# Kernel optimization log

Measured on AMD Instinct MI355X. Metric: run time of the kernel, lower is better.

Reference implementation:

```python
import jax, jax.numpy as jnp
import numpy as np
from jax import lax

B, T, LAT, F2, H = 128, 512, 256, 64, 512
D_IN1 = LAT + F2  # gru5 input dim = 320


def hard_sigmoid(x):
    return jnp.clip(0.2 * x + 0.5, 0.0, 1.0)


def gru_seq(x, W, U, b_in, b_rec, hidden):
    """Keras GRU, reset_after=True, tanh / hard_sigmoid, return_sequences.
    x: [B,T,D], W: [D,3H], U: [H,3H], b_in/b_rec: [3H] -> [B,T,H]."""
    xW = jnp.einsum('btd,dk->btk', x, W) + b_in  # [B,T,3H]
    h0 = jnp.zeros((x.shape[0], hidden), x.dtype)

    def step(h, xt):  # xt: [B,3H]
        inner = h @ U + b_rec
        iz, ir, ih = jnp.split(inner, 3, axis=-1)
        xz, xr, xh = jnp.split(xt, 3, axis=-1)
        zg = hard_sigmoid(xz + iz)
        rg = hard_sigmoid(xr + ir)
        hh = jnp.tanh(xh + rg * ih)
        h_new = zg * h + (1.0 - zg) * hh
        return h_new, h_new

    _, hs = lax.scan(step, h0, jnp.swapaxes(xW, 0, 1))  # [T,B,H]
    return jnp.swapaxes(hs, 0, 1)


def setup_inputs() -> dict:
    key = jax.random.key(0)
    ks = jax.random.split(key, 14)
    s = lambda fan: 1.0 / np.sqrt(fan)
    return {
        'z': jax.random.normal(ks[0], (B, LAT), jnp.float32),
        'train_input_two': jax.random.normal(ks[1], (B, T, F2), jnp.float32),
        'masks': jax.random.uniform(ks[2], (B, T, 1), jnp.float32),
        'dec_masks': jax.random.uniform(ks[3], (B, T, 1), jnp.float32),
        'W5': jax.random.normal(ks[4], (D_IN1, 3 * H), jnp.float32) * s(D_IN1),
        'U5': jax.random.normal(ks[5], (H, 3 * H), jnp.float32) * s(H),
        'bi5': jnp.zeros((3 * H,), jnp.float32),
        'br5': jnp.zeros((3 * H,), jnp.float32),
        'W6': jax.random.normal(ks[6], (H, 3 * H), jnp.float32) * s(H),
        'U6': jax.random.normal(ks[7], (H, 3 * H), jnp.float32) * s(H),
        'bi6': jnp.zeros((3 * H,), jnp.float32),
        'br6': jnp.zeros((3 * H,), jnp.float32),
        'Wd': jax.random.normal(ks[8], (H, 1), jnp.float32) * s(H),
        'bd': jnp.zeros((1,), jnp.float32),
    }


def reference(z, train_input_two, masks, dec_masks,
              W5, U5, bi5, br5, W6, U6, bi6, br6, Wd, bd):
    # RepeatVector: [B,LAT] -> [B,T,LAT]
    rep = jnp.broadcast_to(z[:, None, :], (z.shape[0], T, z.shape[1]))
    concat = jnp.concatenate([rep, train_input_two], axis=-1)  # [B,T,LAT+F2]
    masked = concat * masks                                     # CustomMasking
    g5 = gru_seq(masked, W5, U5, bi5, br5, H)                   # [B,T,H]
    g6 = gru_seq(g5, W6, U6, bi6, br6, H)                       # [B,T,H]
    dec = jnp.tanh(jnp.einsum('bth,ho->bto', g6, Wd) + bd)      # TimeDistributed Dense(1, tanh)
    return dec * dec_masks                                      # [B,T,1]
```

## Files before the change

### kernel.cpp

```cpp
#include <hip/hip_runtime.h>
#include <hip/hip_bf16.h>

typedef unsigned short u16;
typedef unsigned int u32;
typedef unsigned long long u64;
typedef __attribute__((ext_vector_type(8))) short bf16x8;
typedef __attribute__((ext_vector_type(4))) float f32x4;

#define MFMA(a,b,c) __builtin_amdgcn_mfma_f32_16x16x32_bf16((a),(b),(c),0,0,0)
#define AGENT __HIP_MEMORY_SCOPE_AGENT


__device__ __forceinline__ u16 f2bf(float f) {
    u32 u = __float_as_uint(f);
    u32 r = (u + 0x7fffu + ((u >> 16) & 1u)) >> 16;
    return (u16)r;
}
__device__ __forceinline__ float bf2f(u16 v) { return __uint_as_float(((u32)v) << 16); }
__device__ __forceinline__ float sat01(float x) { return fminf(1.f, fmaxf(0.f, x)); }
__device__ __forceinline__ float ftanh(float x) {
    x = fminf(10.f, fmaxf(-10.f, x));
    float e = __expf(2.f * x);
    return (e - 1.f) / (e + 1.f);
}

__device__ __forceinline__ bf16x8 loadB(const float* __restrict__ M, int k0, int colbase,
                                        int l15, int q8) {
    const float* p = M + (size_t)(k0 + q8) * 1536 + colbase + l15;
    bf16x8 r;
#pragma unroll
    for (int j = 0; j < 8; ++j) r[j] = (short)f2bf(p[(size_t)j * 1536]);
    return r;
}

__device__ __forceinline__ bf16x8 ldsA(const u16* s, int stride, int colbase, int l15, int q8) {
    return *(const bf16x8*)(s + l15 * stride + colbase + q8);
}

__global__ void zero_ws_kernel(u32* ws) {
    int i = blockIdx.x * 256 + threadIdx.x;
    if (i < 262400) ws[i] = 0u;
}

__global__ void __launch_bounds__(256, 1)
gru_fused(const float* __restrict__ zin, const float* __restrict__ x2,
          const float* __restrict__ msk, const float* __restrict__ dmsk,
          const float* __restrict__ W5, const float* __restrict__ U5,
          const float* __restrict__ bi5, const float* __restrict__ br5,
          const float* __restrict__ W6, const float* __restrict__ U6,
          const float* __restrict__ bi6, const float* __restrict__ br6,
          const float* __restrict__ Wd, const float* __restrict__ bdp,
          float* __restrict__ out, u32* __restrict__ h5w,
          u32* __restrict__ h6w, u32* __restrict__ cc5)
{
    const int wg = blockIdx.x;
    const bool is6 = wg >= 128;
    const int id = is6 ? wg - 128 : wg;
    const int slice = id & 15;
    const int rgp = id >> 4;
    const int row0 = rgp << 4;
    const int sb = slice << 5;
    const int tid = threadIdx.x;
    const int wv = tid >> 6, lane = tid & 63;
    const int l15 = lane & 15, q8 = (lane >> 4) << 3;

    __shared__ u16 stg[16 * 1032];
    __shared__ float exch[8 * 16 * 17];

    const int ct = wv & 1;
    const int gMain = (wv < 2) ? 0 : 1;
    const int colMain = gMain * 512 + sb + ct * 16;
    const int colH = 1024 + sb + ct * 16;

    const float* bi = is6 ? bi6 : bi5;
    const float* br = is6 ? br6 : br5;
    const float biasM = bi[colMain + l15] + br[colMain + l15];
    const float biasS = (wv < 2) ? bi[colH + l15] : br[colH + l15];

    bf16x8 Bm[32], Bs[16];
    if (!is6) {
#pragma unroll
        for (int kt = 0; kt < 10; ++kt) Bm[kt] = loadB(W5, kt * 32, colMain, l15, q8);
#pragma unroll
        for (int kt = 0; kt < 16; ++kt) Bm[10 + kt] = loadB(U5, kt * 32, colMain, l15, q8);
        if (wv < 2) {
#pragma unroll
            for (int kt = 0; kt < 10; ++kt) Bs[kt] = loadB(W5, kt * 32, colH, l15, q8);
        } else {
#pragma unroll
            for (int kt = 0; kt < 16; ++kt) Bs[kt] = loadB(U5, kt * 32, colH, l15, q8);
        }
    } else {
#pragma unroll
        for (int kt = 0; kt < 16; ++kt) Bm[kt] = loadB(W6, kt * 32, colMain, l15, q8);
#pragma unroll
        for (int kt = 0; kt < 16; ++kt) Bm[16 + kt] = loadB(U6, kt * 32, colMain, l15, q8);
        if (wv < 2) {
#pragma unroll
            for (int kt = 0; kt < 16; ++kt) Bs[kt] = loadB(W6, kt * 32, colH, l15, q8);
        } else {
#pragma unroll
            for (int kt = 0; kt < 16; ++kt) Bs[kt] = loadB(U6, kt * 32, colH, l15, q8);
        }
    }

    float wdv[8]; float bdv = 0.f;
    if (is6 && wv == 0) {
#pragma unroll
        for (int j = 0; j < 8; ++j) wdv[j] = Wd[lane * 8 + j];
        bdv = bdp[0];
    }

    float hold0 = 0.f, hold1 = 0.f;
    const int grow = tid >> 4, cp = tid & 15;
    const int c2p = cp >> 3, ccb = (cp & 7) * 2;

    const int r_ = tid >> 4, cth = tid & 15;
    const int b_ = row0 + r_;

    for (int t = 0; t < 514; ++t) {
        if (!is6) {
            if (t < 512) {
                float mk = msk[b_ * 512 + t];
                for (int c = cth; c < 320; c += 16) {
                    float v = (c < 256) ? zin[b_ * 256 + c]
                                        : x2[(b_ * 512 + t) * 64 + (c - 256)];
                    stg[r_ * 840 + c] = f2bf(v * mk);
                }
                {
                    const u64* src = (const u64*)(h5w + ((t + 1) & 1) * 65536 +
                                                  (size_t)b_ * 512);
                    const u32 exp = (u32)t;
                    u64 v[16];
                    while (true) {
                        bool ok = true;
#pragma unroll
                        for (int k = 0; k < 16; ++k)
                            v[k] = __hip_atomic_load(&src[cth + 16 * k], __ATOMIC_RELAXED, AGENT);
#pragma unroll
                        for (int k = 0; k < 16; ++k) {
                            u32 lo = (u32)v[k], hi = (u32)(v[k] >> 32);
                            if (((lo >> 16) != exp) | ((hi >> 16) != exp)) ok = false;
                        }
                        if (ok) break;
                        __builtin_amdgcn_s_sleep(1);
                    }
                    u16* dst = &stg[r_ * 840 + 320];
#pragma unroll
                    for (int k = 0; k < 16; ++k) {
                        u32 lo = (u32)v[k], hi = (u32)(v[k] >> 32);
                        int c = (cth + 16 * k) * 2;
                        *(u32*)&dst[c] = (lo & 0xffffu) | (hi << 16);
                    }
                }
                __syncthreads();
                f32x4 a0 = {biasM, biasM, biasM, biasM};
                f32x4 a1 = {biasS, biasS, biasS, biasS};
                if (wv < 2) {
#pragma unroll
                    for (int kt = 0; kt < 10; ++kt) {
                        bf16x8 a = ldsA(stg, 840, kt * 32, l15, q8);
                        a0 = MFMA(a, Bm[kt], a0);
                        a1 = MFMA(a, Bs[kt], a1);
                    }
#pragma unroll
                    for (int kt = 0; kt < 16; ++kt) {
                        bf16x8 a = ldsA(stg, 840, 320 + kt * 32, l15, q8);
                        a0 = MFMA(a, Bm[10 + kt], a0);
                    }
                } else {
#pragma unroll
                    for (int kt = 0; kt < 10; ++kt) {
                        bf16x8 a = ldsA(stg, 840, kt * 32, l15, q8);
                        a0 = MFMA(a, Bm[kt], a0);
                    }
#pragma unroll
                    for (int kt = 0; kt < 16; ++kt) {
                        bf16x8 a = ldsA(stg, 840, 320 + kt * 32, l15, q8);
                        a0 = MFMA(a, Bm[10 + kt], a0);
                        a1 = MFMA(a, Bs[kt], a1);
                    }
                }
                {
                    int uM = gMain * 2 + ct, uS = (wv < 2 ? 4 + ct : 6 + ct);
#pragma unroll
                    for (int i = 0; i < 4; ++i) {
                        int rr = (lane >> 4) * 4 + i;
                        exch[uM * 272 + rr * 17 + l15] = a0[i];
                        exch[uS * 272 + rr * 17 + l15] = a1[i];
                    }
                }
                __syncthreads();
                if (t >= 2) {
                    if (tid == 0) {
                        const u32 need = 16u * (u32)(t - 1);
                        while (__hip_atomic_load(&cc5[rgp * 32], __ATOMIC_RELAXED, AGENT) < need)
                            __builtin_amdgcn_s_sleep(1);
                    }
                    __syncthreads();
                }
                {
                    int base0 = (0 + c2p) * 272 + grow * 17 + ccb;
                    int base1 = (2 + c2p) * 272 + grow * 17 + ccb;
                    int base2 = (4 + c2p) * 272 + grow * 17 + ccb;
                    int base3 = (6 + c2p) * 272 + grow * 17 + ccb;
                    float zv0 = exch[base0], zv1 = exch[base0 + 1];
                    float rv0 = exch[base1], rv1 = exch[base1 + 1];
                    float xh0 = exch[base2], xh1 = exch[base2 + 1];
                    float ih0 = exch[base3], ih1 = exch[base3 + 1];
                    float zg0 = sat01(0.2f * zv0 + 0.5f), zg1 = sat01(0.2f * zv1 + 0.5f);
                    float rt0 = sat01(0.2f * rv0 + 0.5f), rt1 = sat01(0.2f * rv1 + 0.5f);
                    float hh0 = ftanh(xh0 + rt0 * ih0), hh1 = ftanh(xh1 + rt1 * ih1);
                    float h0 = zg0 * hold0 + (1.f - zg0) * hh0;
                    float h1 = zg1 * hold1 + (1.f - zg1) * hh1;
                    hold0 = h0; hold1 = h1;
                    const u32 tg = (u32)(t + 1) << 16;
                    u64 w = ((u64)(tg | (u32)f2bf(h1)) << 32) | (u64)(tg | (u32)f2bf(h0));
                    u64* dst = (u64*)(h5w + (t & 1) * 65536 + (size_t)row0 * 512);
                    __hip_atomic_store(&dst[(grow * 512 + sb + cp * 2) >> 1], w,
                                       __ATOMIC_RELAXED, AGENT);
                }
            }
        } else {
            if (t >= 1) {
                const u64* s2 = (const u64*)(h6w + (t & 1) * 65536 + (size_t)b_ * 512);
                const u32 exp2 = (u32)(t - 1);
                if (t <= 512) {
                    const u64* s1 = (const u64*)(h5w + ((t + 1) & 1) * 65536 + (size_t)b_ * 512);
                    const u32 exp1 = (u32)t;
                    u64 v1[16], v2[16];
                    while (true) {
                        bool ok = true;
#pragma unroll
                        for (int k = 0; k < 16; ++k) {
                            v1[k] = __hip_atomic_load(&s1[cth + 16 * k], __ATOMIC_RELAXED, AGENT);
                            v2[k] = __hip_atomic_load(&s2[cth + 16 * k], __ATOMIC_RELAXED, AGENT);
                        }
#pragma unroll
                        for (int k = 0; k < 16; ++k) {
                            u32 lo1 = (u32)v1[k], hi1 = (u32)(v1[k] >> 32);
                            u32 lo2 = (u32)v2[k], hi2 = (u32)(v2[k] >> 32);
                            if (((lo1 >> 16) != exp1) | ((hi1 >> 16) != exp1) |
                                ((lo2 >> 16) != exp2) | ((hi2 >> 16) != exp2)) ok = false;
                        }
                        if (ok) break;
                        __builtin_amdgcn_s_sleep(1);
                    }
#pragma unroll
                    for (int k = 0; k < 16; ++k) {
                        int c = (cth + 16 * k) * 2;
                        u32 lo = (u32)v1[k], hi = (u32)(v1[k] >> 32);
                        *(u32*)&stg[r_ * 1032 + c] = (lo & 0xffffu) | (hi << 16);
                        lo = (u32)v2[k]; hi = (u32)(v2[k] >> 32);
                        *(u32*)&stg[r_ * 1032 + 512 + c] = (lo & 0xffffu) | (hi << 16);
                    }
                } else {
                    u64 v2[16];
                    while (true) {
                        bool ok = true;
#pragma unroll
                        for (int k = 0; k < 16; ++k)
                            v2[k] = __hip_atomic_load(&s2[cth + 16 * k], __ATOMIC_RELAXED, AGENT);
#pragma unroll
                        for (int k = 0; k < 16; ++k) {
                            u32 lo = (u32)v2[k], hi = (u32)(v2[k] >> 32);
                            if (((lo >> 16) != exp2) | ((hi >> 16) != exp2)) ok = false;
                        }
                        if (ok) break;
                        __builtin_amdgcn_s_sleep(1);
                    }
#pragma unroll
                    for (int k = 0; k < 16; ++k) {
                        int c = (cth + 16 * k) * 2;
                        u32 lo = (u32)v2[k], hi = (u32)(v2[k] >> 32);
                        *(u32*)&stg[r_ * 1032 + 512 + c] = (lo & 0xffffu) | (hi << 16);
                    }
                }
            }
            __syncthreads();
            if (t >= 1 && t <= 512 && tid == 0)
                __hip_atomic_fetch_add(&cc5[rgp * 32], 1u, __ATOMIC_RELAXED, AGENT);
            if (t >= 1 && t <= 512) {
                f32x4 a0 = {biasM, biasM, biasM, biasM};
                f32x4 a1 = {biasS, biasS, biasS, biasS};
                if (wv < 2) {
#pragma unroll
                    for (int kt = 0; kt < 16; ++kt) {
                        bf16x8 a = ldsA(stg, 1032, kt * 32, l15, q8);
                        a0 = MFMA(a, Bm[kt], a0);
                        a1 = MFMA(a, Bs[kt], a1);
                    }
#pragma unroll
                    for (int kt = 0; kt < 16; ++kt) {
                        bf16x8 a = ldsA(stg, 1032, 512 + kt * 32, l15, q8);
                        a0 = MFMA(a, Bm[16 + kt], a0);
                    }
                } else {
#pragma unroll
                    for (int kt = 0; kt < 16; ++kt) {
                        bf16x8 a = ldsA(stg, 1032, kt * 32, l15, q8);
                        a0 = MFMA(a, Bm[kt], a0);
                    }
#pragma unroll
                    for (int kt = 0; kt < 16; ++kt) {
                        bf16x8 a = ldsA(stg, 1032, 512 + kt * 32, l15, q8);
                        a0 = MFMA(a, Bm[16 + kt], a0);
                        a1 = MFMA(a, Bs[kt], a1);
                    }
                }
                {
                    int uM = gMain * 2 + ct, uS = (wv < 2 ? 4 + ct : 6 + ct);
#pragma unroll
                    for (int i = 0; i < 4; ++i) {
                        int rr = (lane >> 4) * 4 + i;
                        exch[uM * 272 + rr * 17 + l15] = a0[i];
                        exch[uS * 272 + rr * 17 + l15] = a1[i];
                    }
                }
                __syncthreads();
                {
                    int base0 = (0 + c2p) * 272 + grow * 17 + ccb;
                    int base1 = (2 + c2p) * 272 + grow * 17 + ccb;
                    int base2 = (4 + c2p) * 272 + grow * 17 + ccb;
                    int base3 = (6 + c2p) * 272 + grow * 17 + ccb;
                    float zv0 = exch[base0], zv1 = exch[base0 + 1];
                    float rv0 = exch[base1], rv1 = exch[base1 + 1];
                    float xh0 = exch[base2], xh1 = exch[base2 + 1];
                    float ih0 = exch[base3], ih1 = exch[base3 + 1];
                    float zg0 = sat01(0.2f * zv0 + 0.5f), zg1 = sat01(0.2f * zv1 + 0.5f);
                    float rt0 = sat01(0.2f * rv0 + 0.5f), rt1 = sat01(0.2f * rv1 + 0.5f);
                    float hh0 = ftanh(xh0 + rt0 * ih0), hh1 = ftanh(xh1 + rt1 * ih1);
                    float h0 = zg0 * hold0 + (1.f - zg0) * hh0;
                    float h1 = zg1 * hold1 + (1.f - zg1) * hh1;
                    hold0 = h0; hold1 = h1;
                    const u32 tg = (u32)t << 16;
                    u64 w = ((u64)(tg | (u32)f2bf(h1)) << 32) | (u64)(tg | (u32)f2bf(h0));
                    u64* dst = (u64*)(h6w + ((t + 1) & 1) * 65536 + (size_t)row0 * 512);
                    __hip_atomic_store(&dst[(grow * 512 + sb + cp * 2) >> 1], w,
                                       __ATOMIC_RELAXED, AGENT);
                }
            }
            if (t >= 2 && wv == 0) {
                const u16* hrow = &stg[slice * 1032 + 512 + lane * 8];
                bf16x8 hv = *(const bf16x8*)hrow;
                float s = 0.f;
#pragma unroll
                for (int j = 0; j < 8; ++j) s += bf2f((u16)hv[j]) * wdv[j];
#pragma unroll
                for (int off = 32; off >= 1; off >>= 1) s += __shfl_down(s, off);
                if (lane == 0) {
                    int bb = row0 + slice, tt = t - 2;
                    out[bb * 512 + tt] = ftanh(s + bdv) * dmsk[bb * 512 + tt];
                }
            }
            __syncthreads();
        }
    }
}

extern "C" void kernel_launch(void* const* d_in, const int* in_sizes, int n_in,
                              void* d_out, int out_size, void* d_ws, size_t ws_size,
                              hipStream_t stream) {
    const float* zin = (const float*)d_in[0];
    const float* x2  = (const float*)d_in[1];
    const float* msk = (const float*)d_in[2];
    const float* dmk = (const float*)d_in[3];
    const float* W5  = (const float*)d_in[4];
    const float* U5  = (const float*)d_in[5];
    const float* bi5 = (const float*)d_in[6];
    const float* br5 = (const float*)d_in[7];
    const float* W6  = (const float*)d_in[8];
    const float* U6  = (const float*)d_in[9];
    const float* bi6 = (const float*)d_in[10];
    const float* br6 = (const float*)d_in[11];
    const float* Wd  = (const float*)d_in[12];
    const float* bd  = (const float*)d_in[13];
    float* out = (float*)d_out;

    u32* h5w = (u32*)d_ws;
    u32* h6w = h5w + 131072;
    u32* cc5 = h6w + 131072;

    zero_ws_kernel<<<dim3(1025), dim3(256), 0, stream>>>((u32*)d_ws);

    gru_fused<<<dim3(256), dim3(256), 0, stream>>>(
        zin, x2, msk, dmk, W5, U5, bi5, br5, W6, U6, bi6, br6,
        Wd, bd, out, h5w, h6w, cc5);
}
```

Baseline: 2.357 ms.

## Use 512-thread blocks, fewer workgroups, and per-block sentinel flags for GRU handoff

Each workgroup grows from 256 to 512 threads and covers 64 columns instead of 32, so the grid shrinks from 256 to 128 blocks. The layer-5 state buffer becomes four-deep, and per-block sentinel counters (sent5/sent6) gate reads so consumers spin on one flag rather than polling every tagged element. The decoder dot product moves to shared memory and is split across blocks by row. This is meant to cut per-step cross-workgroup polling and synchronisation cost, at the price of more register and LDS pressure per block and extra flag traffic.

```diff
diff --git a/kernel.cpp b/kernel.cpp
--- a/kernel.cpp
+++ b/kernel.cpp
@@ -39,10 +39,10 @@
 
 __global__ void zero_ws_kernel(u32* ws) {
     int i = blockIdx.x * 256 + threadIdx.x;
-    if (i < 262400) ws[i] = 0u;
-}
-
-__global__ void __launch_bounds__(256, 1)
+    if (i < 397568) ws[i] = 0u;
+}
+
+__global__ void __launch_bounds__(512, 2)
 gru_fused(const float* __restrict__ zin, const float* __restrict__ x2,
           const float* __restrict__ msk, const float* __restrict__ dmsk,
           const float* __restrict__ W5, const float* __restrict__ U5,
@@ -51,138 +51,275 @@
           const float* __restrict__ bi6, const float* __restrict__ br6,
           const float* __restrict__ Wd, const float* __restrict__ bdp,
           float* __restrict__ out, u32* __restrict__ h5w,
-          u32* __restrict__ h6w, u32* __restrict__ cc5)
+          u32* __restrict__ h6w, u32* __restrict__ sent5,
+          u32* __restrict__ sent6, u32* __restrict__ cc5)
 {
     const int wg = blockIdx.x;
-    const bool is6 = wg >= 128;
-    const int id = is6 ? wg - 128 : wg;
-    const int slice = id & 15;
-    const int rgp = id >> 4;
-    const int row0 = rgp << 4;
-    const int sb = slice << 5;
+    const bool is6 = wg >= 64;
+    const int id = is6 ? wg - 64 : wg;
+    const int rg = id >> 3;
+    const int cb = id & 7;
+    const int row0 = rg << 4;
     const int tid = threadIdx.x;
     const int wv = tid >> 6, lane = tid & 63;
     const int l15 = lane & 15, q8 = (lane >> 4) << 3;
+    const int gs = wv >> 2;
+    const int ctl = wv & 3;
 
     __shared__ u16 stg[16 * 1032];
-    __shared__ float exch[8 * 16 * 17];
-
-    const int ct = wv & 1;
-    const int gMain = (wv < 2) ? 0 : 1;
-    const int colMain = gMain * 512 + sb + ct * 16;
-    const int colH = 1024 + sb + ct * 16;
+    __shared__ float exch[16 * 272];
+    __shared__ float wdl[512];
+
+    const int colM = gs * 512 + cb * 64 + ctl * 16;
+    const int colS = 1024 + cb * 64 + ctl * 16;
 
     const float* bi = is6 ? bi6 : bi5;
     const float* br = is6 ? br6 : br5;
-    const float biasM = bi[colMain + l15] + br[colMain + l15];
-    const float biasS = (wv < 2) ? bi[colH + l15] : br[colH + l15];
+    const float biasM = bi[colM + l15] + br[colM + l15];
+    const float biasS = (gs == 0) ? bi[colS + l15] : br[colS + l15];
 
     bf16x8 Bm[32], Bs[16];
+    int nBm, nBs;
     if (!is6) {
 #pragma unroll
-        for (int kt = 0; kt < 10; ++kt) Bm[kt] = loadB(W5, kt * 32, colMain, l15, q8);
-#pragma unroll
-        for (int kt = 0; kt < 16; ++kt) Bm[10 + kt] = loadB(U5, kt * 32, colMain, l15, q8);
-        if (wv < 2) {
-#pragma unroll
-            for (int kt = 0; kt < 10; ++kt) Bs[kt] = loadB(W5, kt * 32, colH, l15, q8);
+        for (int kt = 0; kt < 10; ++kt) Bm[kt] = loadB(W5, kt * 32, colM, l15, q8);
+#pragma unroll
+        for (int kt = 0; kt < 16; ++kt) Bm[10 + kt] = loadB(U5, kt * 32, colM, l15, q8);
+        if (gs == 0) { nBs = 10;
+#pragma unroll
+            for (int kt = 0; kt < 10; ++kt) Bs[kt] = loadB(W5, kt * 32, colS, l15, q8);
+        } else { nBs = 16;
+#pragma unroll
+            for (int kt = 0; kt < 16; ++kt) Bs[kt] = loadB(U5, kt * 32, colS, l15, q8);
+        }
+        nBm = 26;
+    } else {
+#pragma unroll
+        for (int kt = 0; kt < 16; ++kt) Bm[kt] = loadB(W6, kt * 32, colM, l15, q8);
+#pragma unroll
+        for (int kt = 0; kt < 16; ++kt) Bm[16 + kt] = loadB(U6, kt * 32, colM, l15, q8);
+        if (gs == 0) {
+#pragma unroll
+            for (int kt = 0; kt < 16; ++kt) Bs[kt] = loadB(W6, kt * 32, colS, l15, q8);
         } else {
 #pragma unroll
-            for (int kt = 0; kt < 16; ++kt) Bs[kt] = loadB(U5, kt * 32, colH, l15, q8);
+            for (int kt = 0; kt < 16; ++kt) Bs[kt] = loadB(U6, kt * 32, colS, l15, q8);
+        }
+        nBm = 32; nBs = 16;
+        if (tid < 512) wdl[tid] = Wd[tid];
+    }
+    float bdv = bdp[0];
+
+    float hold0 = 0.f, hold1 = 0.f;
+    const int grow = tid & 15, colpair = tid >> 4;
+    const int c0 = colpair * 2, c1 = c0 + 1;
+
+    const int r_ = tid >> 5, cth = tid & 31;
+    const int b_ = row0 + r_;
+
+    if (!is6) {
+        for (int t = 0; t < 512; ++t) {
+            float mk = msk[b_ * 512 + t];
+#pragma unroll
+            for (int i = 0; i < 10; ++i) {
+                int c = cth + 32 * i;
+                float v = (c < 256) ? zin[b_ * 256 + c]
+                                    : x2[(b_ * 512 + t) * 64 + (c - 256)];
+                stg[r_ * 840 + c] = f2bf(v * mk);
+            }
+            if (tid < 8) {
+                while (__hip_atomic_load(&sent5[(rg * 8 + tid) * 32], __ATOMIC_RELAXED, AGENT)
+                       < (u32)t)
+                    __builtin_amdgcn_s_sleep(1);
+            }
+            __syncthreads();
+            {
+                const u64* src = (const u64*)(h5w + ((t + 3) & 3) * 65536) +
+                                 (size_t)b_ * 256;
+                const u32 exp = (u32)t;
+                u64 v[8];
+                for (;;) {
+                    bool ok = true;
+#pragma unroll
+                    for (int k = 0; k < 8; ++k)
+                        v[k] = __hip_atomic_load(&src[cth + 32 * k], __ATOMIC_RELAXED, AGENT);
+#pragma unroll
+                    for (int k = 0; k < 8; ++k) {
+                        u32 lo = (u32)v[k], hi = (u32)(v[k] >> 32);
+                        if (((lo >> 16) != exp) | ((hi >> 16) != exp)) ok = false;
+                    }
+                    if (ok) break;
+                    __builtin_amdgcn_s_sleep(1);
+                }
+#pragma unroll
+                for (int k = 0; k < 8; ++k) {
+                    u32 lo = (u32)v[k], hi = (u32)(v[k] >> 32);
+                    *(u32*)&stg[r_ * 840 + 320 + 2 * (cth + 32 * k)] =
+                        (lo & 0xffffu) | (hi << 16);
+                }
+            }
+            __syncthreads();
+            f32x4 a0 = {biasM, biasM, biasM, biasM};
+            f32x4 a1 = {biasS, biasS, biasS, biasS};
+            if (gs == 0) {
+#pragma unroll
+                for (int kt = 0; kt < 10; ++kt) {
+                    bf16x8 a = ldsA(stg, 840, kt * 32, l15, q8);
+                    a0 = MFMA(a, Bm[kt], a0);
+                    a1 = MFMA(a, Bs[kt], a1);
+                }
+#pragma unroll
+                for (int kt = 0; kt < 16; ++kt) {
+                    bf16x8 a = ldsA(stg, 840, 320 + kt * 32, l15, q8);
+                    a0 = MFMA(a, Bm[10 + kt], a0);
+                }
+            } else {
+#pragma unroll
+                for (int kt = 0; kt < 10; ++kt) {
+                    bf16x8 a = ldsA(stg, 840, kt * 32, l15, q8);
+                    a0 = MFMA(a, Bm[kt], a0);
+                }
+#pragma unroll
+                for (int kt = 0; kt < 16; ++kt) {
+                    bf16x8 a = ldsA(stg, 840, 320 + kt * 32, l15, q8);
+                    a0 = MFMA(a, Bm[10 + kt], a0);
+                    a1 = MFMA(a, Bs[kt], a1);
+                }
+            }
+            {
+                int uM = gs * 4 + ctl, uS = (2 + gs) * 4 + ctl;
+#pragma unroll
+                for (int i = 0; i < 4; ++i) {
+                    int rr = (lane >> 4) * 4 + i;
+                    exch[uM * 272 + rr * 17 + l15] = a0[i];
+                    exch[uS * 272 + rr * 17 + l15] = a1[i];
+                }
+            }
+            __syncthreads();
+            {
+                int t0 = c0 >> 4, cc0 = c0 & 15, t1 = c1 >> 4, cc1 = c1 & 15;
+                float zv0 = exch[(0 + t0) * 272 + grow * 17 + cc0];
+                float zv1 = exch[(0 + t1) * 272 + grow * 17 + cc1];
+                float rv0 = exch[(4 + t0) * 272 + grow * 17 + cc0];
+                float rv1 = exch[(4 + t1) * 272 + grow * 17 + cc1];
+                float xh0 = exch[(8 + t0) * 272 + grow * 17 + cc0];
+                float xh1 = exch[(8 + t1) * 272 + grow * 17 + cc1];
+                float ih0 = exch[(12 + t0) * 272 + grow * 17 + cc0];
+                float ih1 = exch[(12 + t1) * 272 + grow * 17 + cc1];
+                float zg0 = sat01(0.2f * zv0 + 0.5f), zg1 = sat01(0.2f * zv1 + 0.5f);
+                float rt0 = sat01(0.2f * rv0 + 0.5f), rt1 = sat01(0.2f * rv1 + 0.5f);
+                float hh0 = ftanh(xh0 + rt0 * ih0), hh1 = ftanh(xh1 + rt1 * ih1);
+                float h0 = zg0 * hold0 + (1.f - zg0) * hh0;
+                float h1 = zg1 * hold1 + (1.f - zg1) * hh1;
+                hold0 = h0; hold1 = h1;
+                if (t >= 4) {
+                    const u32 need = 8u * (u32)(t - 3);
+                    while (__hip_atomic_load(&cc5[rg * 32], __ATOMIC_RELAXED, AGENT) < need)
+                        __builtin_amdgcn_s_sleep(1);
+                }
+                const u32 tg = (u32)(t + 1) << 16;
+                u64 w = ((u64)(tg | (u32)f2bf(h1)) << 32) | (u64)(tg | (u32)f2bf(h0));
+                u64* dst = (u64*)(h5w + (t & 3) * 65536) + (size_t)(row0 + grow) * 256;
+                __hip_atomic_store(&dst[(cb * 64 + c0) >> 1], w, __ATOMIC_RELAXED, AGENT);
+            }
+            __syncthreads();
+            if (tid == 0)
+                __hip_atomic_store(&sent5[(rg * 8 + cb) * 32], (u32)(t + 1),
+                                   __ATOMIC_RELAXED, AGENT);
         }
     } else {
-#pragma unroll
-        for (int kt = 0; kt < 16; ++kt) Bm[kt] = loadB(W6, kt * 32, colMain, l15, q8);
-#pragma unroll
-        for (int kt = 0; kt < 16; ++kt) Bm[16 + kt] = loadB(U6, kt * 32, colMain, l15, q8);
-        if (wv < 2) {
-#pragma unroll
-            for (int kt = 0; kt < 16; ++kt) Bs[kt] = loadB(W6, kt * 32, colH, l15, q8);
-        } else {
-#pragma unroll
-            for (int kt = 0; kt < 16; ++kt) Bs[kt] = loadB(U6, kt * 32, colH, l15, q8);
-        }
-    }
-
-    float wdv[8]; float bdv = 0.f;
-    if (is6 && wv == 0) {
-#pragma unroll
-        for (int j = 0; j < 8; ++j) wdv[j] = Wd[lane * 8 + j];
-        bdv = bdp[0];
-    }
-
-    float hold0 = 0.f, hold1 = 0.f;
-    const int grow = tid >> 4, cp = tid & 15;
-    const int c2p = cp >> 3, ccb = (cp & 7) * 2;
-
-    const int r_ = tid >> 4, cth = tid & 15;
-    const int b_ = row0 + r_;
-
-    for (int t = 0; t < 514; ++t) {
-        if (!is6) {
-            if (t < 512) {
-                float mk = msk[b_ * 512 + t];
-                for (int c = cth; c < 320; c += 16) {
-                    float v = (c < 256) ? zin[b_ * 256 + c]
-                                        : x2[(b_ * 512 + t) * 64 + (c - 256)];
-                    stg[r_ * 840 + c] = f2bf(v * mk);
-                }
-                {
-                    const u64* src = (const u64*)(h5w + ((t + 1) & 1) * 65536 +
-                                                  (size_t)b_ * 512);
-                    const u32 exp = (u32)t;
-                    u64 v[16];
-                    while (true) {
-                        bool ok = true;
-#pragma unroll
-                        for (int k = 0; k < 16; ++k)
-                            v[k] = __hip_atomic_load(&src[cth + 16 * k], __ATOMIC_RELAXED, AGENT);
-#pragma unroll
-                        for (int k = 0; k < 16; ++k) {
-                            u32 lo = (u32)v[k], hi = (u32)(v[k] >> 32);
-                            if (((lo >> 16) != exp) | ((hi >> 16) != exp)) ok = false;
-                        }
-                        if (ok) break;
-                        __builtin_amdgcn_s_sleep(1);
-                    }
-                    u16* dst = &stg[r_ * 840 + 320];
-#pragma unroll
-                    for (int k = 0; k < 16; ++k) {
+        for (int t = 1; t <= 513; ++t) {
+            if (t <= 512 && tid < 8) {
+                while (__hip_atomic_load(&sent5[(rg * 8 + tid) * 32], __ATOMIC_RELAXED, AGENT)
+                       < (u32)t)
+                    __builtin_amdgcn_s_sleep(1);
+            }
+            if (tid >= 64 && tid < 72) {
+                while (__hip_atomic_load(&sent6[(rg * 8 + tid - 64) * 32], __ATOMIC_RELAXED, AGENT)
+                       < (u32)(t - 1))
+                    __builtin_amdgcn_s_sleep(1);
+            }
+            __syncthreads();
+            if (t <= 512) {
+                const u64* s1 = (const u64*)(h5w + ((t + 3) & 3) * 65536) + (size_t)b_ * 256;
+                const u32 exp = (u32)t;
+                u64 v[8];
+                for (;;) {
+                    bool ok = true;
+#pragma unroll
+                    for (int k = 0; k < 8; ++k)
+                        v[k] = __hip_atomic_load(&s1[cth + 32 * k], __ATOMIC_RELAXED, AGENT);
+#pragma unroll
+                    for (int k = 0; k < 8; ++k) {
                         u32 lo = (u32)v[k], hi = (u32)(v[k] >> 32);
-                        int c = (cth + 16 * k) * 2;
-                        *(u32*)&dst[c] = (lo & 0xffffu) | (hi << 16);
-                    }
-                }
-                __syncthreads();
+                        if (((lo >> 16) != exp) | ((hi >> 16) != exp)) ok = false;
+                    }
+                    if (ok) break;
+                    __builtin_amdgcn_s_sleep(1);
+                }
+#pragma unroll
+                for (int k = 0; k < 8; ++k) {
+                    u32 lo = (u32)v[k], hi = (u32)(v[k] >> 32);
+                    *(u32*)&stg[r_ * 1032 + 2 * (cth + 32 * k)] = (lo & 0xffffu) | (hi << 16);
+                }
+            }
+            {
+                const u64* s2 = (const u64*)(h6w + (t & 1) * 65536) + (size_t)b_ * 256;
+                const u32 exp = (u32)(t - 1);
+                u64 v[8];
+                for (;;) {
+                    bool ok = true;
+#pragma unroll
+                    for (int k = 0; k < 8; ++k)
+                        v[k] = __hip_atomic_load(&s2[cth + 32 * k], __ATOMIC_RELAXED, AGENT);
+#pragma unroll
+                    for (int k = 0; k < 8; ++k) {
+                        u32 lo = (u32)v[k], hi = (u32)(v[k] >> 32);
+                        if (((lo >> 16) != exp) | ((hi >> 16) != exp)) ok = false;
+                    }
+                    if (ok) break;
+                    __builtin_amdgcn_s_sleep(1);
+                }
+#pragma unroll
+                for (int k = 0; k < 8; ++k) {
+                    u32 lo = (u32)v[k], hi = (u32)(v[k] >> 32);
+                    *(u32*)&stg[r_ * 1032 + 512 + 2 * (cth + 32 * k)] =
+                        (lo & 0xffffu) | (hi << 16);
+                }
+            }
+            __syncthreads();
+            if (t <= 512 && tid == 0)
+                __hip_atomic_fetch_add(&cc5[rg * 32], 1u, __ATOMIC_RELAXED, AGENT);
+            if (t <= 512) {
                 f32x4 a0 = {biasM, biasM, biasM, biasM};
                 f32x4 a1 = {biasS, biasS, biasS, biasS};
-                if (wv < 2) {
-#pragma unroll
-                    for (int kt = 0; kt < 10; ++kt) {
-                        bf16x8 a = ldsA(stg, 840, kt * 32, l15, q8);
+                if (gs == 0) {
+#pragma unroll
+                    for (int kt = 0; kt < 16; ++kt) {
+                        bf16x8 a = ldsA(stg, 1032, kt * 32, l15, q8);
                         a0 = MFMA(a, Bm[kt], a0);
                         a1 = MFMA(a, Bs[kt], a1);
                     }
 #pragma unroll
                     for (int kt = 0; kt < 16; ++kt) {
-                        bf16x8 a = ldsA(stg, 840, 320 + kt * 32, l15, q8);
-                        a0 = MFMA(a, Bm[10 + kt], a0);
+                        bf16x8 a = ldsA(stg, 1032, 512 + kt * 32, l15, q8);
+                        a0 = MFMA(a, Bm[16 + kt], a0);
                     }
                 } else {
 #pragma unroll
-                    for (int kt = 0; kt < 10; ++kt) {
-                        bf16x8 a = ldsA(stg, 840, kt * 32, l15, q8);
+                    for (int kt = 0; kt < 16; ++kt) {
+                        bf16x8 a = ldsA(stg, 1032, kt * 32, l15, q8);
                         a0 = MFMA(a, Bm[kt], a0);
                     }
 #pragma unroll
                     for (int kt = 0; kt < 16; ++kt) {
-                        bf16x8 a = ldsA(stg, 840, 320 + kt * 32, l15, q8);
-                        a0 = MFMA(a, Bm[10 + kt], a0);
+                        bf16x8 a = ldsA(stg, 1032, 512 + kt * 32, l15, q8);
+                        a0 = MFMA(a, Bm[16 + kt], a0);
                         a1 = MFMA(a, Bs[kt], a1);
                     }
                 }
                 {
-                    int uM = gMain * 2 + ct, uS = (wv < 2 ? 4 + ct : 6 + ct);
+                    int uM = gs * 4 + ctl, uS = (2 + gs) * 4 + ctl;
 #pragma unroll
                     for (int i = 0; i < 4; ++i) {
                         int rr = (lane >> 4) * 4 + i;
@@ -191,142 +328,16 @@
                     }
                 }
                 __syncthreads();
-                if (t >= 2) {
-                    if (tid == 0) {
-                        const u32 need = 16u * (u32)(t - 1);
-                        while (__hip_atomic_load(&cc5[rgp * 32], __ATOMIC_RELAXED, AGENT) < need)
-                            __builtin_amdgcn_s_sleep(1);
-                    }
-                    __syncthreads();
-                }
                 {
-                    int base0 = (0 + c2p) * 272 + grow * 17 + ccb;
-                    int base1 = (2 + c2p) * 272 + grow * 17 + ccb;
-                    int base2 = (4 + c2p) * 272 + grow * 17 + ccb;
-                    int base3 = (6 + c2p) * 272 + grow * 17 + ccb;
-                    float zv0 = exch[base0], zv1 = exch[base0 + 1];
-                    float rv0 = exch[base1], rv1 = exch[base1 + 1];
-                    float xh0 = exch[base2], xh1 = exch[base2 + 1];
-                    float ih0 = exch[base3], ih1 = exch[base3 + 1];
-                    float zg0 = sat01(0.2f * zv0 + 0.5f), zg1 = sat01(0.2f * zv1 + 0.5f);
-                    float rt0 = sat01(0.2f * rv0 + 0.5f), rt1 = sat01(0.2f * rv1 + 0.5f);
-                    float hh0 = ftanh(xh0 + rt0 * ih0), hh1 = ftanh(xh1 + rt1 * ih1);
-                    float h0 = zg0 * hold0 + (1.f - zg0) * hh0;
-                    float h1 = zg1 * hold1 + (1.f - zg1) * hh1;
-                    hold0 = h0; hold1 = h1;
-                    const u32 tg = (u32)(t + 1) << 16;
-                    u64 w = ((u64)(tg | (u32)f2bf(h1)) << 32) | (u64)(tg | (u32)f2bf(h0));
-                    u64* dst = (u64*)(h5w + (t & 1) * 65536 + (size_t)row0 * 512);
-                    __hip_atomic_store(&dst[(grow * 512 + sb + cp * 2) >> 1], w,
-                                       __ATOMIC_RELAXED, AGENT);
-                }
-            }
-        } else {
-            if (t >= 1) {
-                const u64* s2 = (const u64*)(h6w + (t & 1) * 65536 + (size_t)b_ * 512);
-                const u32 exp2 = (u32)(t - 1);
-                if (t <= 512) {
-                    const u64* s1 = (const u64*)(h5w + ((t + 1) & 1) * 65536 + (size_t)b_ * 512);
-                    const u32 exp1 = (u32)t;
-                    u64 v1[16], v2[16];
-                    while (true) {
-                        bool ok = true;
-#pragma unroll
-                        for (int k = 0; k < 16; ++k) {
-                            v1[k] = __hip_atomic_load(&s1[cth + 16 * k], __ATOMIC_RELAXED, AGENT);
-                            v2[k] = __hip_atomic_load(&s2[cth + 16 * k], __ATOMIC_RELAXED, AGENT);
-                        }
-#pragma unroll
-                        for (int k = 0; k < 16; ++k) {
-                            u32 lo1 = (u32)v1[k], hi1 = (u32)(v1[k] >> 32);
-                            u32 lo2 = (u32)v2[k], hi2 = (u32)(v2[k] >> 32);
-                            if (((lo1 >> 16) != exp1) | ((hi1 >> 16) != exp1) |
-                                ((lo2 >> 16) != exp2) | ((hi2 >> 16) != exp2)) ok = false;
-                        }
-                        if (ok) break;
-                        __builtin_amdgcn_s_sleep(1);
-                    }
-#pragma unroll
-                    for (int k = 0; k < 16; ++k) {
-                        int c = (cth + 16 * k) * 2;
-                        u32 lo = (u32)v1[k], hi = (u32)(v1[k] >> 32);
-                        *(u32*)&stg[r_ * 1032 + c] = (lo & 0xffffu) | (hi << 16);
-                        lo = (u32)v2[k]; hi = (u32)(v2[k] >> 32);
-                        *(u32*)&stg[r_ * 1032 + 512 + c] = (lo & 0xffffu) | (hi << 16);
-                    }
-                } else {
-                    u64 v2[16];
-                    while (true) {
-                        bool ok = true;
-#pragma unroll
-                        for (int k = 0; k < 16; ++k)
-                            v2[k] = __hip_atomic_load(&s2[cth + 16 * k], __ATOMIC_RELAXED, AGENT);
-#pragma unroll
-                        for (int k = 0; k < 16; ++k) {
-                            u32 lo = (u32)v2[k], hi = (u32)(v2[k] >> 32);
-                            if (((lo >> 16) != exp2) | ((hi >> 16) != exp2)) ok = false;
-                        }
-                        if (ok) break;
-                        __builtin_amdgcn_s_sleep(1);
-                    }
-#pragma unroll
-                    for (int k = 0; k < 16; ++k) {
-                        int c = (cth + 16 * k) * 2;
-                        u32 lo = (u32)v2[k], hi = (u32)(v2[k] >> 32);
-                        *(u32*)&stg[r_ * 1032 + 512 + c] = (lo & 0xffffu) | (hi << 16);
-                    }
-                }
-            }
-            __syncthreads();
-            if (t >= 1 && t <= 512 && tid == 0)
-                __hip_atomic_fetch_add(&cc5[rgp * 32], 1u, __ATOMIC_RELAXED, AGENT);
-            if (t >= 1 && t <= 512) {
-                f32x4 a0 = {biasM, biasM, biasM, biasM};
-                f32x4 a1 = {biasS, biasS, biasS, biasS};
-                if (wv < 2) {
-#pragma unroll
-                    for (int kt = 0; kt < 16; ++kt) {
-                        bf16x8 a = ldsA(stg, 1032, kt * 32, l15, q8);
-                        a0 = MFMA(a, Bm[kt], a0);
-                        a1 = MFMA(a, Bs[kt], a1);
-                    }
-#pragma unroll
-                    for (int kt = 0; kt < 16; ++kt) {
-                        bf16x8 a = ldsA(stg, 1032, 512 + kt * 32, l15, q8);
-                        a0 = MFMA(a, Bm[16 + kt], a0);
-                    }
-                } else {
-#pragma unroll
-                    for (int kt = 0; kt < 16; ++kt) {
-                        bf16x8 a = ldsA(stg, 1032, kt * 32, l15, q8);
-                        a0 = MFMA(a, Bm[kt], a0);
-                    }
-#pragma unroll
-                    for (int kt = 0; kt < 16; ++kt) {
-                        bf16x8 a = ldsA(stg, 1032, 512 + kt * 32, l15, q8);
-                        a0 = MFMA(a, Bm[16 + kt], a0);
-                        a1 = MFMA(a, Bs[kt], a1);
-                    }
-                }
-                {
-                    int uM = gMain * 2 + ct, uS = (wv < 2 ? 4 + ct : 6 + ct);
-#pragma unroll
-                    for (int i = 0; i < 4; ++i) {
-                        int rr = (lane >> 4) * 4 + i;
-                        exch[uM * 272 + rr * 17 + l15] = a0[i];
-                        exch[uS * 272 + rr * 17 + l15] = a1[i];
-                    }
-                }
-                __syncthreads();
-                {
-                    int base0 = (0 + c2p) * 272 + grow * 17 + ccb;
-                    int base1 = (2 + c2p) * 272 + grow * 17 + ccb;
-                    int base2 = (4 + c2p) * 272 + grow * 17 + ccb;
-                    int base3 = (6 + c2p) * 272 + grow * 17 + ccb;
-                    float zv0 = exch[base0], zv1 = exch[base0 + 1];
-                    float rv0 = exch[base1], rv1 = exch[base1 + 1];
-                    float xh0 = exch[base2], xh1 = exch[base2 + 1];
-                    float ih0 = exch[base3], ih1 = exch[base3 + 1];
+                    int t0 = c0 >> 4, cc0 = c0 & 15, t1 = c1 >> 4, cc1 = c1 & 15;
+                    float zv0 = exch[(0 + t0) * 272 + grow * 17 + cc0];
+                    float zv1 = exch[(0 + t1) * 272 + grow * 17 + cc1];
+                    float rv0 = exch[(4 + t0) * 272 + grow * 17 + cc0];
+                    float rv1 = exch[(4 + t1) * 272 + grow * 17 + cc1];
+                    float xh0 = exch[(8 + t0) * 272 + grow * 17 + cc0];
+                    float xh1 = exch[(8 + t1) * 272 + grow * 17 + cc1];
+                    float ih0 = exch[(12 + t0) * 272 + grow * 17 + cc0];
+                    float ih1 = exch[(12 + t1) * 272 + grow * 17 + cc1];
                     float zg0 = sat01(0.2f * zv0 + 0.5f), zg1 = sat01(0.2f * zv1 + 0.5f);
                     float rt0 = sat01(0.2f * rv0 + 0.5f), rt1 = sat01(0.2f * rv1 + 0.5f);
                     float hh0 = ftanh(xh0 + rt0 * ih0), hh1 = ftanh(xh1 + rt1 * ih1);
@@ -335,25 +346,30 @@
                     hold0 = h0; hold1 = h1;
                     const u32 tg = (u32)t << 16;
                     u64 w = ((u64)(tg | (u32)f2bf(h1)) << 32) | (u64)(tg | (u32)f2bf(h0));
-                    u64* dst = (u64*)(h6w + ((t + 1) & 1) * 65536 + (size_t)row0 * 512);
-                    __hip_atomic_store(&dst[(grow * 512 + sb + cp * 2) >> 1], w,
-                                       __ATOMIC_RELAXED, AGENT);
+                    u64* dst = (u64*)(h6w + ((t + 1) & 1) * 65536) + (size_t)(row0 + grow) * 256;
+                    __hip_atomic_store(&dst[(cb * 64 + c0) >> 1], w, __ATOMIC_RELAXED, AGENT);
                 }
             }
             if (t >= 2 && wv == 0) {
-                const u16* hrow = &stg[slice * 1032 + 512 + lane * 8];
-                bf16x8 hv = *(const bf16x8*)hrow;
+                int rw = lane >> 5;
+                int rdec = 2 * cb + rw;
+                int kb = (lane & 31) * 16;
                 float s = 0.f;
 #pragma unroll
-                for (int j = 0; j < 8; ++j) s += bf2f((u16)hv[j]) * wdv[j];
-#pragma unroll
-                for (int off = 32; off >= 1; off >>= 1) s += __shfl_down(s, off);
-                if (lane == 0) {
-                    int bb = row0 + slice, tt = t - 2;
+                for (int j = 0; j < 16; ++j)
+                    s += bf2f(stg[rdec * 1032 + 512 + kb + j]) * wdl[kb + j];
+#pragma unroll
+                for (int off = 16; off >= 1; off >>= 1)
+                    s += __shfl_down(s, off, 32);
+                if ((lane & 31) == 0) {
+                    int bb = row0 + rdec, tt = t - 2;
                     out[bb * 512 + tt] = ftanh(s + bdv) * dmsk[bb * 512 + tt];
                 }
             }
             __syncthreads();
+            if (t <= 512 && tid == 0)
+                __hip_atomic_store(&sent6[(rg * 8 + cb) * 32], (u32)t,
+                                   __ATOMIC_RELAXED, AGENT);
         }
     }
 }
@@ -378,12 +394,14 @@
     float* out = (float*)d_out;
 
     u32* h5w = (u32*)d_ws;
-    u32* h6w = h5w + 131072;
-    u32* cc5 = h6w + 131072;
-
-    zero_ws_kernel<<<dim3(1025), dim3(256), 0, stream>>>((u32*)d_ws);
-
-    gru_fused<<<dim3(256), dim3(256), 0, stream>>>(
+    u32* h6w = h5w + 262144;
+    u32* sent5 = h6w + 131072;
+    u32* sent6 = sent5 + 2048;
+    u32* cc5 = sent6 + 2048;
+
+    zero_ws_kernel<<<dim3(1553), dim3(256), 0, stream>>>((u32*)d_ws);
+
+    gru_fused<<<dim3(128), dim3(512), 0, stream>>>(
         zin, x2, msk, dmk, W5, U5, bi5, br5, W6, U6, bi6, br6,
-        Wd, bd, out, h5w, h6w, cc5);
-}
+        Wd, bd, out, h5w, h6w, sent5, sent6, cc5);
+}
```

Result: slower. 4.085 ms (+73.3%).

## Deepen hidden-state ring to four slots and overlap input GEMM with polling

Applied to the files above, without the earlier changes.

Expands the h5/h6 exchange buffers from double to quad buffering, which loosens the back-pressure wait on the layer-6 consumer counter (now t-3 instead of t-1). The layer-5 input-projection MFMAs now run before waiting on the recurrent state, so the x·W part overlaps the inter-block latency. Polling becomes per-element spin loops instead of whole-vector retry loops, and the layer-6 blocks poll h6 and h5 separately. The workspace and zeroing kernel double in size, and correctness depends on the new slot indexing matching between producers and consumers.

```diff
diff --git a/kernel.cpp b/kernel.cpp
--- a/kernel.cpp
+++ b/kernel.cpp
@@ -39,7 +39,7 @@
 
 __global__ void zero_ws_kernel(u32* ws) {
     int i = blockIdx.x * 256 + threadIdx.x;
-    if (i < 262400) ws[i] = 0u;
+    if (i < 524544) ws[i] = 0u;
 }
 
 __global__ void __launch_bounds__(256, 1)
@@ -118,169 +118,142 @@
     const int r_ = tid >> 4, cth = tid & 15;
     const int b_ = row0 + r_;
 
-    for (int t = 0; t < 514; ++t) {
-        if (!is6) {
-            if (t < 512) {
-                float mk = msk[b_ * 512 + t];
-                for (int c = cth; c < 320; c += 16) {
-                    float v = (c < 256) ? zin[b_ * 256 + c]
-                                        : x2[(b_ * 512 + t) * 64 + (c - 256)];
-                    stg[r_ * 840 + c] = f2bf(v * mk);
-                }
-                {
-                    const u64* src = (const u64*)(h5w + ((t + 1) & 1) * 65536 +
-                                                  (size_t)b_ * 512);
-                    const u32 exp = (u32)t;
-                    u64 v[16];
-                    while (true) {
-                        bool ok = true;
-#pragma unroll
-                        for (int k = 0; k < 16; ++k)
-                            v[k] = __hip_atomic_load(&src[cth + 16 * k], __ATOMIC_RELAXED, AGENT);
-#pragma unroll
-                        for (int k = 0; k < 16; ++k) {
-                            u32 lo = (u32)v[k], hi = (u32)(v[k] >> 32);
-                            if (((lo >> 16) != exp) | ((hi >> 16) != exp)) ok = false;
-                        }
-                        if (ok) break;
+    if (!is6) {
+        for (int t = 0; t < 512; ++t) {
+            const u64* src = (const u64*)(h5w + ((t + 3) & 3) * 65536) + (size_t)b_ * 256;
+            const u32 exp = (u32)t;
+            u64 v[16];
+#pragma unroll
+            for (int k = 0; k < 16; ++k)
+                v[k] = __hip_atomic_load(&src[cth + 16 * k], __ATOMIC_RELAXED, AGENT);
+            float mk = msk[b_ * 512 + t];
+            for (int c = cth; c < 320; c += 16) {
+                float xv = (c < 256) ? zin[b_ * 256 + c]
+                                     : x2[(b_ * 512 + t) * 64 + (c - 256)];
+                stg[r_ * 840 + c] = f2bf(xv * mk);
+            }
+            __syncthreads();
+            f32x4 a0 = {biasM, biasM, biasM, biasM};
+            f32x4 a1 = {biasS, biasS, biasS, biasS};
+            if (wv < 2) {
+#pragma unroll
+                for (int kt = 0; kt < 10; ++kt) {
+                    bf16x8 a = ldsA(stg, 840, kt * 32, l15, q8);
+                    a0 = MFMA(a, Bm[kt], a0);
+                    a1 = MFMA(a, Bs[kt], a1);
+                }
+            } else {
+#pragma unroll
+                for (int kt = 0; kt < 10; ++kt) {
+                    bf16x8 a = ldsA(stg, 840, kt * 32, l15, q8);
+                    a0 = MFMA(a, Bm[kt], a0);
+                }
+            }
+#pragma unroll
+            for (int k = 0; k < 16; ++k) {
+                u32 lo = (u32)v[k], hi = (u32)(v[k] >> 32);
+                while (((lo >> 16) != exp) | ((hi >> 16) != exp)) {
+                    __builtin_amdgcn_s_sleep(1);
+                    u64 nv = __hip_atomic_load(&src[cth + 16 * k], __ATOMIC_RELAXED, AGENT);
+                    lo = (u32)nv; hi = (u32)(nv >> 32);
+                }
+                *(u32*)&stg[r_ * 840 + 320 + 2 * (cth + 16 * k)] = (lo & 0xffffu) | (hi << 16);
+            }
+            __syncthreads();
+            if (wv < 2) {
+#pragma unroll
+                for (int kt = 0; kt < 16; ++kt) {
+                    bf16x8 a = ldsA(stg, 840, 320 + kt * 32, l15, q8);
+                    a0 = MFMA(a, Bm[10 + kt], a0);
+                }
+            } else {
+#pragma unroll
+                for (int kt = 0; kt < 16; ++kt) {
+                    bf16x8 a = ldsA(stg, 840, 320 + kt * 32, l15, q8);
+                    a0 = MFMA(a, Bm[10 + kt], a0);
+                    a1 = MFMA(a, Bs[kt], a1);
+                }
+            }
+            {
+                int uM = gMain * 2 + ct, uS = (wv < 2 ? 4 + ct : 6 + ct);
+#pragma unroll
+                for (int i = 0; i < 4; ++i) {
+                    int rr = (lane >> 4) * 4 + i;
+                    exch[uM * 272 + rr * 17 + l15] = a0[i];
+                    exch[uS * 272 + rr * 17 + l15] = a1[i];
+                }
+            }
+            __syncthreads();
+            {
+                int base0 = (0 + c2p) * 272 + grow * 17 + ccb;
+                int base1 = (2 + c2p) * 272 + grow * 17 + ccb;
+                int base2 = (4 + c2p) * 272 + grow * 17 + ccb;
+                int base3 = (6 + c2p) * 272 + grow * 17 + ccb;
+                float zv0 = exch[base0], zv1 = exch[base0 + 1];
+                float rv0 = exch[base1], rv1 = exch[base1 + 1];
+                float xh0 = exch[base2], xh1 = exch[base2 + 1];
+                float ih0 = exch[base3], ih1 = exch[base3 + 1];
+                float zg0 = sat01(0.2f * zv0 + 0.5f), zg1 = sat01(0.2f * zv1 + 0.5f);
+                float rt0 = sat01(0.2f * rv0 + 0.5f), rt1 = sat01(0.2f * rv1 + 0.5f);
+                float hh0 = ftanh(xh0 + rt0 * ih0), hh1 = ftanh(xh1 + rt1 * ih1);
+                float h0 = zg0 * hold0 + (1.f - zg0) * hh0;
+                float h1 = zg1 * hold1 + (1.f - zg1) * hh1;
+                hold0 = h0; hold1 = h1;
+                if (t >= 4) {
+                    const u32 need = 16u * (u32)(t - 3);
+                    while (__hip_atomic_load(&cc5[rgp * 32], __ATOMIC_RELAXED, AGENT) < need)
                         __builtin_amdgcn_s_sleep(1);
-                    }
-                    u16* dst = &stg[r_ * 840 + 320];
-#pragma unroll
-                    for (int k = 0; k < 16; ++k) {
-                        u32 lo = (u32)v[k], hi = (u32)(v[k] >> 32);
-                        int c = (cth + 16 * k) * 2;
-                        *(u32*)&dst[c] = (lo & 0xffffu) | (hi << 16);
-                    }
-                }
-                __syncthreads();
-                f32x4 a0 = {biasM, biasM, biasM, biasM};
-                f32x4 a1 = {biasS, biasS, biasS, biasS};
-                if (wv < 2) {
-#pragma unroll
-                    for (int kt = 0; kt < 10; ++kt) {
-                        bf16x8 a = ldsA(stg, 840, kt * 32, l15, q8);
-                        a0 = MFMA(a, Bm[kt], a0);
-                        a1 = MFMA(a, Bs[kt], a1);
-                    }
-#pragma unroll
-                    for (int kt = 0; kt < 16; ++kt) {
-                        bf16x8 a = ldsA(stg, 840, 320 + kt * 32, l15, q8);
-                        a0 = MFMA(a, Bm[10 + kt], a0);
-                    }
-                } else {
-#pragma unroll
-                    for (int kt = 0; kt < 10; ++kt) {
-                        bf16x8 a = ldsA(stg, 840, kt * 32, l15, q8);
-                        a0 = MFMA(a, Bm[kt], a0);
-                    }
-#pragma unroll
-                    for (int kt = 0; kt < 16; ++kt) {
-                        bf16x8 a = ldsA(stg, 840, 320 + kt * 32, l15, q8);
-                        a0 = MFMA(a, Bm[10 + kt], a0);
-                        a1 = MFMA(a, Bs[kt], a1);
-                    }
-                }
-                {
-                    int uM = gMain * 2 + ct, uS = (wv < 2 ? 4 + ct : 6 + ct);
-#pragma unroll
-                    for (int i = 0; i < 4; ++i) {
-                        int rr = (lane >> 4) * 4 + i;
-                        exch[uM * 272 + rr * 17 + l15] = a0[i];
-                        exch[uS * 272 + rr * 17 + l15] = a1[i];
-                    }
-                }
-                __syncthreads();
-                if (t >= 2) {
-                    if (tid == 0) {
-                        const u32 need = 16u * (u32)(t - 1);
-                        while (__hip_atomic_load(&cc5[rgp * 32], __ATOMIC_RELAXED, AGENT) < need)
-                            __builtin_amdgcn_s_sleep(1);
-                    }
-                    __syncthreads();
-                }
-                {
-                    int base0 = (0 + c2p) * 272 + grow * 17 + ccb;
-                    int base1 = (2 + c2p) * 272 + grow * 17 + ccb;
-                    int base2 = (4 + c2p) * 272 + grow * 17 + ccb;
-                    int base3 = (6 + c2p) * 272 + grow * 17 + ccb;
-                    float zv0 = exch[base0], zv1 = exch[base0 + 1];
-                    float rv0 = exch[base1], rv1 = exch[base1 + 1];
-                    float xh0 = exch[base2], xh1 = exch[base2 + 1];
-                    float ih0 = exch[base3], ih1 = exch[base3 + 1];
-                    float zg0 = sat01(0.2f * zv0 + 0.5f), zg1 = sat01(0.2f * zv1 + 0.5f);
-                    float rt0 = sat01(0.2f * rv0 + 0.5f), rt1 = sat01(0.2f * rv1 + 0.5f);
-                    float hh0 = ftanh(xh0 + rt0 * ih0), hh1 = ftanh(xh1 + rt1 * ih1);
-                    float h0 = zg0 * hold0 + (1.f - zg0) * hh0;
-                    float h1 = zg1 * hold1 + (1.f - zg1) * hh1;
-                    hold0 = h0; hold1 = h1;
-                    const u32 tg = (u32)(t + 1) << 16;
-                    u64 w = ((u64)(tg | (u32)f2bf(h1)) << 32) | (u64)(tg | (u32)f2bf(h0));
-                    u64* dst = (u64*)(h5w + (t & 1) * 65536 + (size_t)row0 * 512);
-                    __hip_atomic_store(&dst[(grow * 512 + sb + cp * 2) >> 1], w,
-                                       __ATOMIC_RELAXED, AGENT);
-                }
-            }
-        } else {
-            if (t >= 1) {
-                const u64* s2 = (const u64*)(h6w + (t & 1) * 65536 + (size_t)b_ * 512);
+                }
+                const u32 tg = (u32)(t + 1) << 16;
+                u64 w = ((u64)(tg | (u32)f2bf(h1)) << 32) | (u64)(tg | (u32)f2bf(h0));
+                u64* dst = (u64*)(h5w + (t & 3) * 65536);
+                __hip_atomic_store(&dst[((row0 + grow) * 512 + sb + cp * 2) >> 1], w,
+                                   __ATOMIC_RELAXED, AGENT);
+            }
+        }
+    } else {
+        for (int t = 1; t <= 513; ++t) {
+            {
+                const u64* s2 = (const u64*)(h6w + ((t + 2) & 3) * 65536) + (size_t)b_ * 256;
                 const u32 exp2 = (u32)(t - 1);
-                if (t <= 512) {
-                    const u64* s1 = (const u64*)(h5w + ((t + 1) & 1) * 65536 + (size_t)b_ * 512);
-                    const u32 exp1 = (u32)t;
-                    u64 v1[16], v2[16];
-                    while (true) {
-                        bool ok = true;
-#pragma unroll
-                        for (int k = 0; k < 16; ++k) {
-                            v1[k] = __hip_atomic_load(&s1[cth + 16 * k], __ATOMIC_RELAXED, AGENT);
-                            v2[k] = __hip_atomic_load(&s2[cth + 16 * k], __ATOMIC_RELAXED, AGENT);
-                        }
-#pragma unroll
-                        for (int k = 0; k < 16; ++k) {
-                            u32 lo1 = (u32)v1[k], hi1 = (u32)(v1[k] >> 32);
-                            u32 lo2 = (u32)v2[k], hi2 = (u32)(v2[k] >> 32);
-                            if (((lo1 >> 16) != exp1) | ((hi1 >> 16) != exp1) |
-                                ((lo2 >> 16) != exp2) | ((hi2 >> 16) != exp2)) ok = false;
-                        }
-                        if (ok) break;
+                u64 v[16];
+#pragma unroll
+                for (int k = 0; k < 16; ++k)
+                    v[k] = __hip_atomic_load(&s2[cth + 16 * k], __ATOMIC_RELAXED, AGENT);
+#pragma unroll
+                for (int k = 0; k < 16; ++k) {
+                    u32 lo = (u32)v[k], hi = (u32)(v[k] >> 32);
+                    while (((lo >> 16) != exp2) | ((hi >> 16) != exp2)) {
                         __builtin_amdgcn_s_sleep(1);
-                    }
-#pragma unroll
-                    for (int k = 0; k < 16; ++k) {
-                        int c = (cth + 16 * k) * 2;
-                        u32 lo = (u32)v1[k], hi = (u32)(v1[k] >> 32);
-                        *(u32*)&stg[r_ * 1032 + c] = (lo & 0xffffu) | (hi << 16);
-                        lo = (u32)v2[k]; hi = (u32)(v2[k] >> 32);
-                        *(u32*)&stg[r_ * 1032 + 512 + c] = (lo & 0xffffu) | (hi << 16);
-                    }
-                } else {
-                    u64 v2[16];
-                    while (true) {
-                        bool ok = true;
-#pragma unroll
-                        for (int k = 0; k < 16; ++k)
-                            v2[k] = __hip_atomic_load(&s2[cth + 16 * k], __ATOMIC_RELAXED, AGENT);
-#pragma unroll
-                        for (int k = 0; k < 16; ++k) {
-                            u32 lo = (u32)v2[k], hi = (u32)(v2[k] >> 32);
-                            if (((lo >> 16) != exp2) | ((hi >> 16) != exp2)) ok = false;
-                        }
-                        if (ok) break;
+                        u64 nv = __hip_atomic_load(&s2[cth + 16 * k], __ATOMIC_RELAXED, AGENT);
+                        lo = (u32)nv; hi = (u32)(nv >> 32);
+                    }
+                    *(u32*)&stg[r_ * 1032 + 512 + 2 * (cth + 16 * k)] =
+                        (lo & 0xffffu) | (hi << 16);
+                }
+            }
+            if (t <= 512) {
+                const u64* s1 = (const u64*)(h5w + ((t + 3) & 3) * 65536) + (size_t)b_ * 256;
+                const u32 exp1 = (u32)t;
+                u64 v[16];
+#pragma unroll
+                for (int k = 0; k < 16; ++k)
+                    v[k] = __hip_atomic_load(&s1[cth + 16 * k], __ATOMIC_RELAXED, AGENT);
+#pragma unroll
+                for (int k = 0; k < 16; ++k) {
+                    u32 lo = (u32)v[k], hi = (u32)(v[k] >> 32);
+                    while (((lo >> 16) != exp1) | ((hi >> 16) != exp1)) {
                         __builtin_amdgcn_s_sleep(1);
-                    }
-#pragma unroll
-                    for (int k = 0; k < 16; ++k) {
-                        int c = (cth + 16 * k) * 2;
-                        u32 lo = (u32)v2[k], hi = (u32)(v2[k] >> 32);
-                        *(u32*)&stg[r_ * 1032 + 512 + c] = (lo & 0xffffu) | (hi << 16);
-                    }
-                }
-            }
-            __syncthreads();
-            if (t >= 1 && t <= 512 && tid == 0)
+                        u64 nv = __hip_atomic_load(&s1[cth + 16 * k], __ATOMIC_RELAXED, AGENT);
+                        lo = (u32)nv; hi = (u32)(nv >> 32);
+                    }
+                    *(u32*)&stg[r_ * 1032 + 2 * (cth + 16 * k)] = (lo & 0xffffu) | (hi << 16);
+                }
+            }
+            __syncthreads();
+            if (t <= 512 && tid == 0)
                 __hip_atomic_fetch_add(&cc5[rgp * 32], 1u, __ATOMIC_RELAXED, AGENT);
-            if (t >= 1 && t <= 512) {
+            if (t <= 512) {
                 f32x4 a0 = {biasM, biasM, biasM, biasM};
                 f32x4 a1 = {biasS, biasS, biasS, biasS};
                 if (wv < 2) {
@@ -335,8 +308,8 @@
                     hold0 = h0; hold1 = h1;
                     const u32 tg = (u32)t << 16;
                     u64 w = ((u64)(tg | (u32)f2bf(h1)) << 32) | (u64)(tg | (u32)f2bf(h0));
-                    u64* dst = (u64*)(h6w + ((t + 1) & 1) * 65536 + (size_t)row0 * 512);
-                    __hip_atomic_store(&dst[(grow * 512 + sb + cp * 2) >> 1], w,
+                    u64* dst = (u64*)(h6w + ((t + 3) & 3) * 65536);
+                    __hip_atomic_store(&dst[((row0 + grow) * 512 + sb + cp * 2) >> 1], w,
                                        __ATOMIC_RELAXED, AGENT);
                 }
             }
@@ -378,10 +351,10 @@
     float* out = (float*)d_out;
 
     u32* h5w = (u32*)d_ws;
-    u32* h6w = h5w + 131072;
-    u32* cc5 = h6w + 131072;
-
-    zero_ws_kernel<<<dim3(1025), dim3(256), 0, stream>>>((u32*)d_ws);
+    u32* h6w = h5w + 262144;
+    u32* cc5 = h6w + 262144;
+
+    zero_ws_kernel<<<dim3(2049), dim3(256), 0, stream>>>((u32*)d_ws);
 
     gru_fused<<<dim3(256), dim3(256), 0, stream>>>(
         zin, x2, msk, dmk, W5, U5, bi5, br5, W6, U6, bi6, br6,
```

Result: slower. 3.207 ms (+36.1%).
